# Kernel tuning notes

Measured on AMD Instinct MI355X. Metric: run time of the kernel, lower is better.

## Reference

```python
import jax, jax.numpy as jnp
import numpy as np
from jax import lax

B, C, H, W = 8, 384, 64, 64


def cos_map(N):
    # ortho DCT-II basis: weight[n, x] = cos(n*(x+0.5)*pi/N) * sqrt(2/N), row 0 /= sqrt(2)
    wx = (jnp.arange(N, dtype=jnp.float32) + 0.5) / N
    wn = jnp.arange(N, dtype=jnp.float32)[:, None]
    w = jnp.cos(wn * wx[None, :] * jnp.pi) * np.sqrt(2.0 / N).astype(np.float32)
    return w.at[0, :].multiply(np.float32(1.0 / np.sqrt(2.0)))


def setup_inputs() -> dict:
    key = jax.random.key(0)
    ks = jax.random.split(key, 8)
    s = 0.05
    return {
        "x": jax.random.normal(ks[0], (B, C, H, W), jnp.float32),
        "freq_embed": jax.random.normal(ks[1], (H, W, C), jnp.float32),
        "dw_w": jax.random.normal(ks[2], (C, 1, 3, 3), jnp.float32) * s,
        "dw_b": jnp.zeros((C,), jnp.float32),
        "lin_w": jax.random.normal(ks[3], (2 * C, C), jnp.float32) * s,
        "lin_b": jnp.zeros((2 * C,), jnp.float32),
        "tok_w": jax.random.normal(ks[4], (C, C), jnp.float32) * s,
        "tok_b": jnp.zeros((C,), jnp.float32),
        "c": jnp.ones((1,), jnp.float32),
        "alpha": jnp.ones((1,), jnp.float32) * 0.1,
        "ln_g": jnp.ones((C,), jnp.float32),
        "ln_b": jnp.zeros((C,), jnp.float32),
        "out_w": jax.random.normal(ks[5], (C, C), jnp.float32) * s,
        "out_b": jnp.zeros((C,), jnp.float32),
    }


def reference(x, freq_embed, dw_w, dw_b, lin_w, lin_b, tok_w, tok_b, c, alpha, ln_g, ln_b, out_w, out_b):
    Bc, Cc, Hc, Wc = x.shape
    # depthwise 3x3 conv
    x = lax.conv_general_dilated(x, dw_w, (1, 1), 'SAME',
                                 feature_group_count=Cc,
                                 dimension_numbers=('NCHW', 'OIHW', 'NCHW'))
    x = x + dw_b[None, :, None, None]
    # linear to 2C (channels-last), split into signal x and gate z
    xz = jnp.einsum('bchw,dc->bhwd', x, lin_w) + lin_b
    xs, z = xz[..., :Cc], xz[..., Cc:]          # [B,H,W,C]
    xs = jnp.transpose(xs, (0, 3, 1, 2))        # [B,C,H,W]
    # 2D ortho DCT-II: D = Wh @ x @ Ww^T
    Wh, Ww = cos_map(Hc), cos_map(Wc)
    Xd = jnp.einsum('nh,bchw,kw->bcnk', Wh, xs, Ww)
    # learned frequency gating: t = ReLU(Linear(freq_embed)), per (H,W,C)
    t = jax.nn.relu(jnp.einsum('hwc,dc->hwd', freq_embed, tok_w) + tok_b)
    ct = jnp.transpose(jnp.cos(c * t), (2, 0, 1))[None]        # [1,C,H,W]
    st = jnp.transpose(jnp.sin(c * t), (2, 0, 1))[None] / c[0]
    # x_u0 == x_v0 == Xd in the original (dct2d applied twice to same x)
    final = ct * Xd + st * (Xd + 0.5 * alpha[0] * Xd)
    # 2D inverse DCT: x = Wh^T @ D @ Ww
    xi = jnp.einsum('nh,bcnk,kw->bchw', Wh, final, Ww)
    # LayerNorm over channels, gate with SiLU(z), output linear
    y = jnp.transpose(xi, (0, 2, 3, 1))          # [B,H,W,C]
    mu = jnp.mean(y, axis=-1, keepdims=True)
    var = jnp.mean((y - mu) ** 2, axis=-1, keepdims=True)
    y = (y - mu) * lax.rsqrt(var + 1e-5) * ln_g + ln_b
    y = y * jax.nn.silu(z)
    y = jnp.einsum('bhwc,dc->bhwd', y, out_w) + out_b
    return jnp.transpose(y, (0, 3, 1, 2))        # [B,C,H,W]
```

## Files before the change

kernel.cpp:

```cpp
#include <hip/hip_runtime.h>

typedef _Float16 h2 __attribute__((ext_vector_type(2)));
typedef _Float16 h4 __attribute__((ext_vector_type(4)));
typedef _Float16 h8 __attribute__((ext_vector_type(8)));
typedef float    f4 __attribute__((ext_vector_type(4)));

#define MFMA32(a,b,c) __builtin_amdgcn_mfma_f32_16x16x32_f16((a),(b),(c),0,0,0)
#define MFMA16(a,b,c) __builtin_amdgcn_mfma_f32_16x16x16f16((a),(b),(c),0,0,0)

#define B_N 8
#define C_N 384
#define P_N 4096
#define PI_F 3.14159265358979323846f

__device__ __forceinline__ h4 to_h4(f4 v) {
  h4 r; r[0]=(_Float16)v[0]; r[1]=(_Float16)v[1]; r[2]=(_Float16)v[2]; r[3]=(_Float16)v[3];
  return r;
}

__device__ __forceinline__ void gl_lds16(const _Float16* g, _Float16* l) {
  __builtin_amdgcn_global_load_lds(
      (const __attribute__((address_space(1))) void*)g,
      (__attribute__((address_space(3))) void*)l, 16, 0, 0);
}

__global__ __launch_bounds__(256) void k_setup(
    const float* __restrict__ lin_w, const float* __restrict__ tok_w,
    const float* __restrict__ out_w, _Float16* __restrict__ lwh,
    _Float16* __restrict__ twh, _Float16* __restrict__ owh,
    _Float16* __restrict__ wmg, _Float16* __restrict__ wmtg) {
  int t = blockIdx.x * 256 + threadIdx.x;
  if (t < 768*384) lwh[t] = (_Float16)lin_w[t];
  if (t < 384*384) { twh[t] = (_Float16)tok_w[t]; owh[t] = (_Float16)out_w[t]; }
  if (t < 4096) {
    int n = t >> 6, h = t & 63;
    float v = cosf((float)n * ((float)h + 0.5f) * (PI_F / 64.0f)) * 0.1767766952966369f;
    if (n == 0) v *= 0.7071067811865476f;
    wmg[n*64 + h]  = (_Float16)v;
    wmtg[h*64 + n] = (_Float16)v;
  }
}

__global__ __launch_bounds__(256) void k_dwconv(
    const float* __restrict__ x, const float* __restrict__ dww,
    const float* __restrict__ dwb, _Float16* __restrict__ xdw) {
  int blk = blockIdx.x;
  int h = blk & 63;
  int rest = blk >> 6;
  int cgi = rest % 6;
  int b = rest / 6;
  int c0 = cgi * 64;
  int t = threadIdx.x;
  int w = t & 63, ci = t >> 6;
  __shared__ _Float16 buf[64 * 68];
  const float* xb = x + (size_t)b * C_N * P_N;
  int wl = (w > 0)  ? w - 1 : 0;
  int wr = (w < 63) ? w + 1 : 63;
  #pragma unroll
  for (int j = 0; j < 8; j++) {
    int lc = ci * 16 + j * 2;
    h2 pr;
    #pragma unroll
    for (int e = 0; e < 2; e++) {
      int c = c0 + lc + e;
      const float* xc = xb + (size_t)c * P_N;
      float k0=dww[c*9+0],k1=dww[c*9+1],k2=dww[c*9+2];
      float k3=dww[c*9+3],k4=dww[c*9+4],k5=dww[c*9+5];
      float k6=dww[c*9+6],k7=dww[c*9+7],k8=dww[c*9+8];
      float top = (h > 0)  ? xc[(h-1)*64 + w] : 0.0f;
      float mid = xc[h*64 + w];
      float bot = (h < 63) ? xc[(h+1)*64 + w] : 0.0f;
      float tl = __shfl(top, wl, 64), tr = __shfl(top, wr, 64);
      float ml = __shfl(mid, wl, 64), mr = __shfl(mid, wr, 64);
      float bl = __shfl(bot, wl, 64), br = __shfl(bot, wr, 64);
      if (w == 0)  { tl = 0.f; ml = 0.f; bl = 0.f; }
      if (w == 63) { tr = 0.f; mr = 0.f; br = 0.f; }
      float acc = dwb[c];
      acc += k0*tl + k1*top + k2*tr;
      acc += k3*ml + k4*mid + k5*mr;
      acc += k6*bl + k7*bot + k8*br;
      pr[e] = (_Float16)acc;
    }
    *(h2*)&buf[w*68 + lc] = pr;
  }
  __syncthreads();
  _Float16* op = xdw + ((size_t)b*P_N + h*64) * C_N + c0;
  #pragma unroll
  for (int i = 0; i < 4; i++) {
    int flat = (t + 256*i) * 4;
    int pix = flat >> 6, cl = flat & 63;
    *(h4*)&op[(size_t)pix*C_N + cl] = *(const h4*)&buf[pix*68 + cl];
  }
}

__global__ __launch_bounds__(256) void k_gate(
    const float* __restrict__ fe, const _Float16* __restrict__ twh,
    const float* __restrict__ tkb, const float* __restrict__ cc,
    const float* __restrict__ aa, _Float16* __restrict__ g) {
  int pt = blockIdx.x & 63, dt = blockIdx.x >> 6;
  int p0 = pt*64, d0 = dt*64;
  int t = threadIdx.x, lane = t & 63, wave = t >> 6;
  int quad = lane >> 4, l15 = lane & 15;
  int wm_ = wave >> 1, wn = wave & 1;
  __shared__ _Float16 la[64*40], lb[64*40];
  int srow = t >> 2, scg = (t & 3) * 8;
  f4 acc[2][2] = {};
  for (int kc = 0; kc < 384; kc += 32) {
    const float* src = fe + (size_t)(p0 + srow)*384 + kc + scg;
    f4 v0 = *(const f4*)src;
    f4 v1 = *(const f4*)(src + 4);
    h8 hv;
    hv[0]=(_Float16)v0[0]; hv[1]=(_Float16)v0[1]; hv[2]=(_Float16)v0[2]; hv[3]=(_Float16)v0[3];
    hv[4]=(_Float16)v1[0]; hv[5]=(_Float16)v1[1]; hv[6]=(_Float16)v1[2]; hv[7]=(_Float16)v1[3];
    *(h8*)&la[srow*40 + scg] = hv;
    *(h8*)&lb[srow*40 + scg] = *(const h8*)&twh[(size_t)(d0 + srow)*384 + kc + scg];
    __syncthreads();
    h8 a0 = *(const h8*)&la[(wm_*32 + l15)*40 + quad*8];
    h8 a1 = *(const h8*)&la[(wm_*32 + 16 + l15)*40 + quad*8];
    h8 b0 = *(const h8*)&lb[(wn*32 + l15)*40 + quad*8];
    h8 b1 = *(const h8*)&lb[(wn*32 + 16 + l15)*40 + quad*8];
    acc[0][0] = MFMA32(a0, b0, acc[0][0]);
    acc[0][1] = MFMA32(a0, b1, acc[0][1]);
    acc[1][0] = MFMA32(a1, b0, acc[1][0]);
    acc[1][1] = MFMA32(a1, b1, acc[1][1]);
    __syncthreads();
  }
  float c0 = cc[0];
  float s1 = (1.0f + 0.5f*aa[0]) / c0;
  #pragma unroll
  for (int i = 0; i < 2; i++)
  #pragma unroll
  for (int j = 0; j < 2; j++) {
    int d  = d0 + wn*32 + j*16 + l15;
    int pl = wm_*32 + i*16 + quad*4;
    float bias = tkb[d];
    h4 hv;
    #pragma unroll
    for (int r = 0; r < 4; r++) {
      float tv = fmaxf(acc[i][j][r] + bias, 0.0f);
      hv[r] = (_Float16)(__cosf(c0*tv) + s1*__sinf(c0*tv));
    }
    *(h4*)&g[(size_t)d*P_N + p0 + pl] = hv;
  }
}

__global__ __launch_bounds__(256) void k_gemm1(
    const _Float16* __restrict__ xdw, const _Float16* __restrict__ lwh,
    const float* __restrict__ lnb, _Float16* __restrict__ xs,
    _Float16* __restrict__ zs) {
  int pt = blockIdx.x & 31;
  int rest = blockIdx.x >> 5;
  int dt = rest % 6, b = rest / 6;
  int p0 = pt * 128, d0 = dt * 128;
  int t = threadIdx.x, lane = t & 63, wave = t >> 6;
  int quad = lane >> 4, l15 = lane & 15;
  int wm = wave >> 1, wn = wave & 1;
  __shared__ _Float16 la[128 * 32];
  __shared__ _Float16 lb[128 * 32];
  int s_row = lane >> 2;
  int s_col = (lane & 3) * 8;
  const _Float16* ga = xdw + ((size_t)b*P_N + p0) * 384 + s_col;
  const _Float16* gb = lwh + (size_t)d0 * 384 + s_col;
  f4 acc[4][4] = {};
  for (int kc = 0; kc < 384; kc += 32) {
    #pragma unroll
    for (int s = 0; s < 2; s++) {
      int seg = wave * 2 + s;
      int row = seg * 16 + s_row;
      gl_lds16(ga + (size_t)row*384 + kc, &la[seg*512 + lane*8]);
      gl_lds16(gb + (size_t)row*384 + kc, &lb[seg*512 + lane*8]);
    }
    __syncthreads();
    h8 af[4], bf[4];
    #pragma unroll
    for (int i = 0; i < 4; i++) {
      af[i] = *(const h8*)&la[(wm*64 + i*16 + l15)*32 + quad*8];
      bf[i] = *(const h8*)&lb[(wn*64 + i*16 + l15)*32 + quad*8];
    }
    #pragma unroll
    for (int i = 0; i < 4; i++)
    #pragma unroll
    for (int j = 0; j < 4; j++)
      acc[i][j] = MFMA32(af[i], bf[j], acc[i][j]);
    __syncthreads();
  }
  bool isz = (d0 >= 384);
  #pragma unroll
  for (int j = 0; j < 4; j++) {
    int d = d0 + wn*64 + j*16 + l15;
    float bias = lnb[d];
    _Float16* dst = isz ? (zs + ((size_t)b*C_N + (d-384)) * P_N)
                        : (xs + ((size_t)b*C_N + d) * P_N);
    #pragma unroll
    for (int i = 0; i < 4; i++) {
      int p = p0 + wm*64 + i*16 + quad*4;
      h4 hv;
      if (isz) {
        #pragma unroll
        for (int r = 0; r < 4; r++) {
          float v = acc[i][j][r] + bias;
          v = v / (1.0f + __expf(-v));
          hv[r] = (_Float16)v;
        }
      } else {
        #pragma unroll
        for (int r = 0; r < 4; r++) hv[r] = (_Float16)(acc[i][j][r] + bias);
      }
      *(h4*)&dst[p] = hv;
    }
  }
}

__global__ __launch_bounds__(256) void k_dct(
    const _Float16* __restrict__ xs, const _Float16* __restrict__ g,
    const _Float16* __restrict__ wmg, const _Float16* __restrict__ wmtg,
    _Float16* __restrict__ xi) {
  int b = blockIdx.x / 96, cg = blockIdx.x % 96;
  int c0 = cg * 4;
  int t = threadIdx.x, wave = t >> 6, lane = t & 63;
  int quad = lane >> 4, l15 = lane & 15;
  __shared__ _Float16 wm_s[64*72];
  __shared__ _Float16 wmt_s[64*72];
  __shared__ _Float16 pb[4][64*72];
  for (int i = t; i < 512; i += 256) {
    int row = i >> 3, col = (i & 7) * 8;
    *(h8*)&wm_s[row*72 + col]  = *(const h8*)&wmg[row*64 + col];
    *(h8*)&wmt_s[row*72 + col] = *(const h8*)&wmtg[row*64 + col];
  }
  const _Float16* xsb = xs + ((size_t)b*C_N + c0) * P_N;
  for (int i = t; i < 2048; i += 256) {
    int pl = i >> 9, idx = i & 511;
    int p = idx * 8, hh = p >> 6, ww = p & 63;
    *(h8*)&pb[pl][hh*72 + ww] = *(const h8*)&xsb[(size_t)pl*P_N + p];
  }
  __syncthreads();
  h8 aS[4][2], bW[4][2];
  #pragma unroll
  for (int I = 0; I < 4; I++)
  #pragma unroll
  for (int kk = 0; kk < 2; kk++) {
    aS[I][kk] = *(const h8*)&pb[wave][(I*16 + l15)*72 + kk*32 + quad*8];
    bW[I][kk] = *(const h8*)&wm_s[(I*16 + l15)*72 + kk*32 + quad*8];
  }
  h4 t1h[4][4];
  #pragma unroll
  for (int I = 0; I < 4; I++)
  #pragma unroll
  for (int J = 0; J < 4; J++) {
    f4 a = {};
    a = MFMA32(aS[I][0], bW[J][0], a);
    a = MFMA32(aS[I][1], bW[J][1], a);
    t1h[I][J] = to_h4(a);
  }
  __syncthreads();
  const _Float16* gb = g + (size_t)c0 * P_N;
  for (int i = t; i < 2048; i += 256) {
    int pl = i >> 9, idx = i & 511;
    int p = idx * 8, hh = p >> 6, ww = p & 63;
    *(h8*)&pb[pl][hh*72 + ww] = *(const h8*)&gb[(size_t)pl*P_N + p];
  }
  __syncthreads();
  f4 t2[4][4] = {};
  #pragma unroll
  for (int I = 0; I < 4; I++)
  #pragma unroll
  for (int K4 = 0; K4 < 4; K4++) {
    h4 af = *(const h4*)&wm_s[(I*16 + l15)*72 + K4*16 + quad*4];
    #pragma unroll
    for (int J = 0; J < 4; J++) t2[I][J] = MFMA16(af, t1h[K4][J], t2[I][J]);
  }
  h4 fh[4][4];
  #pragma unroll
  for (int I = 0; I < 4; I++)
  #pragma unroll
  for (int J = 0; J < 4; J++) {
    int n0 = I*16 + quad*4, k = J*16 + l15;
    h4 r;
    #pragma unroll
    for (int rr = 0; rr < 4; rr++) {
      float gv = (float)pb[wave][(n0+rr)*72 + k];
      r[rr] = (_Float16)(t2[I][J][rr] * gv);
    }
    fh[I][J] = r;
  }
  f4 t3[4][4] = {};
  #pragma unroll
  for (int J = 0; J < 4; J++)
  #pragma unroll
  for (int K4 = 0; K4 < 4; K4++) {
    h4 bf = *(const h4*)&wmt_s[(J*16 + l15)*72 + K4*16 + quad*4];
    #pragma unroll
    for (int I = 0; I < 4; I++) t3[I][J] = MFMA16(fh[K4][I], bf, t3[I][J]);
  }
  h4 t3h[4][4];
  #pragma unroll
  for (int I = 0; I < 4; I++)
  #pragma unroll
  for (int J = 0; J < 4; J++) t3h[I][J] = to_h4(t3[I][J]);
  f4 t4[4][4] = {};
  #pragma unroll
  for (int I = 0; I < 4; I++)
  #pragma unroll
  for (int K4 = 0; K4 < 4; K4++) {
    h4 af = *(const h4*)&wmt_s[(I*16 + l15)*72 + K4*16 + quad*4];
    #pragma unroll
    for (int J = 0; J < 4; J++) t4[I][J] = MFMA16(af, t3h[K4][J], t4[I][J]);
  }
  #pragma unroll
  for (int I = 0; I < 4; I++)
  #pragma unroll
  for (int J = 0; J < 4; J++) {
    int w0 = I*16 + quad*4, hq = J*16 + l15;
    *(h4*)&pb[wave][hq*72 + w0] = to_h4(t4[I][J]);
  }
  __syncthreads();
  _Float16* xib = xi + ((size_t)b*C_N + c0) * P_N;
  for (int i = t; i < 2048; i += 256) {
    int pl = i >> 9, idx = i & 511;
    int p = idx * 8, hh = p >> 6, ww = p & 63;
    *(h8*)&xib[(size_t)pl*P_N + p] = *(const h8*)&pb[pl][hh*72 + ww];
  }
}

__global__ __launch_bounds__(256) void k_ubuild(
    const _Float16* __restrict__ xi, const _Float16* __restrict__ zs,
    const float* __restrict__ lng, const float* __restrict__ lnbv,
    _Float16* __restrict__ u) {
  int b = blockIdx.x >> 6, pt = blockIdx.x & 63;
  int p0 = pt * 64;
  int t = threadIdx.x;
  __shared__ _Float16 ut[64 * 392];
  __shared__ float red[4][64], red2[4][64];
  __shared__ float muL[64], rsL[64];
  int cr = t >> 3;
  int px0 = (t & 7) * 8;
  const _Float16* xib = xi + (size_t)b * C_N * P_N;
  #pragma unroll
  for (int i = 0; i < 12; i++) {
    int c = cr + 32 * i;
    h8 v = *(const h8*)&xib[(size_t)c * P_N + p0 + px0];
    #pragma unroll
    for (int e = 0; e < 8; e++) ut[(px0 + e) * 392 + c] = v[e];
  }
  __syncthreads();
  int px = t & 63, seg = t >> 6;
  float s = 0.f, ss = 0.f;
  #pragma unroll
  for (int j = 0; j < 12; j++) {
    h8 v = *(const h8*)&ut[px * 392 + seg * 96 + j * 8];
    #pragma unroll
    for (int e = 0; e < 8; e++) { float f = (float)v[e]; s += f; ss += f * f; }
  }
  red[seg][px] = s; red2[seg][px] = ss;
  __syncthreads();
  if (t < 64) {
    float st  = red[0][t] + red[1][t] + red[2][t] + red[3][t];
    float sst = red2[0][t] + red2[1][t] + red2[2][t] + red2[3][t];
    float m = st * (1.f/384.f);
    float var = sst * (1.f/384.f) - m * m;
    muL[t] = m; rsL[t] = rsqrtf(var + 1e-5f);
  }
  __syncthreads();
  const _Float16* zb = zs + (size_t)b * C_N * P_N;
  #pragma unroll
  for (int i = 0; i < 12; i++) {
    int c = cr + 32 * i;
    float g = lng[c], bb = lnbv[c];
    h8 zv = *(const h8*)&zb[(size_t)c * P_N + p0 + px0];
    #pragma unroll
    for (int e = 0; e < 8; e++) {
      int p = px0 + e;
      float y = ((float)ut[p * 392 + c] - muL[p]) * rsL[p] * g + bb;
      ut[p * 392 + c] = (_Float16)(y * (float)zv[e]);
    }
  }
  __syncthreads();
  _Float16* ub = u + ((size_t)b * P_N + p0) * C_N;
  #pragma unroll
  for (int i = 0; i < 12; i++) {
    int idx = t + 256 * i;
    int row = idx / 48, ch = idx % 48;
    *(h8*)&ub[(size_t)row * C_N + ch * 8] = *(const h8*)&ut[row * 392 + ch * 8];
  }
}

__global__ __launch_bounds__(256) void k_gemm2(
    const _Float16* __restrict__ u, const _Float16* __restrict__ owh,
    const float* __restrict__ ob, float* __restrict__ out) {
  int pt = blockIdx.x & 31;
  int rest = blockIdx.x >> 5;
  int dt = rest % 3, b = rest / 3;
  int p0 = pt * 128, d0 = dt * 128;
  int t = threadIdx.x, lane = t & 63, wave = t >> 6;
  int quad = lane >> 4, l15 = lane & 15;
  int wm = wave >> 1, wn = wave & 1;
  __shared__ _Float16 la[128 * 32];
  __shared__ _Float16 lb[128 * 32];
  int s_row = lane >> 2;
  int s_col = (lane & 3) * 8;
  const _Float16* ga = u   + ((size_t)b*P_N + p0) * 384 + s_col;
  const _Float16* gb = owh + (size_t)d0 * 384 + s_col;
  f4 acc[4][4] = {};
  for (int kc = 0; kc < 384; kc += 32) {
    #pragma unroll
    for (int s = 0; s < 2; s++) {
      int seg = wave * 2 + s;
      int row = seg * 16 + s_row;
      gl_lds16(ga + (size_t)row*384 + kc, &la[seg*512 + lane*8]);
      gl_lds16(gb + (size_t)row*384 + kc, &lb[seg*512 + lane*8]);
    }
    __syncthreads();
    h8 af[4], bf[4];
    #pragma unroll
    for (int i = 0; i < 4; i++) {
      af[i] = *(const h8*)&la[(wm*64 + i*16 + l15)*32 + quad*8];
      bf[i] = *(const h8*)&lb[(wn*64 + i*16 + l15)*32 + quad*8];
    }
    #pragma unroll
    for (int i = 0; i < 4; i++)
    #pragma unroll
    for (int j = 0; j < 4; j++)
      acc[i][j] = MFMA32(af[i], bf[j], acc[i][j]);
    __syncthreads();
  }
  #pragma unroll
  for (int j = 0; j < 4; j++) {
    int d = d0 + wn*64 + j*16 + l15;
    float bias = ob[d];
    #pragma unroll
    for (int i = 0; i < 4; i++) {
      int p = p0 + wm*64 + i*16 + quad*4;
      f4 v;
      #pragma unroll
      for (int r = 0; r < 4; r++) v[r] = acc[i][j][r] + bias;
      *(f4*)&out[((size_t)b*C_N + d)*P_N + p] = v;
    }
  }
}

extern "C" void kernel_launch(void* const* d_in, const int* in_sizes, int n_in,
                              void* d_out, int out_size, void* d_ws, size_t ws_size,
                              hipStream_t stream) {
  (void)in_sizes; (void)n_in; (void)out_size; (void)ws_size;
  const float* x    = (const float*)d_in[0];
  const float* fe   = (const float*)d_in[1];
  const float* dww  = (const float*)d_in[2];
  const float* dwb  = (const float*)d_in[3];
  const float* linw = (const float*)d_in[4];
  const float* linb = (const float*)d_in[5];
  const float* tokw = (const float*)d_in[6];
  const float* tokb = (const float*)d_in[7];
  const float* cc   = (const float*)d_in[8];
  const float* aa   = (const float*)d_in[9];
  const float* lng  = (const float*)d_in[10];
  const float* lnbv = (const float*)d_in[11];
  const float* outw = (const float*)d_in[12];
  const float* outb = (const float*)d_in[13];
  float* out = (float*)d_out;

  char* ws = (char*)d_ws;
  size_t off = 0;
  auto alloc = [&](size_t bytes) -> void* {
    void* p = ws + off;
    off += (bytes + 255) & ~(size_t)255;
    return p;
  };
  _Float16* lwh  = (_Float16*)alloc((size_t)768*384*2);
  _Float16* twh  = (_Float16*)alloc((size_t)384*384*2);
  _Float16* owh  = (_Float16*)alloc((size_t)384*384*2);
  _Float16* wmg  = (_Float16*)alloc((size_t)64*64*2);
  _Float16* wmtg = (_Float16*)alloc((size_t)64*64*2);
  _Float16* xdw  = (_Float16*)alloc((size_t)B_N*P_N*C_N*2);
  _Float16* xs   = (_Float16*)alloc((size_t)B_N*C_N*P_N*2);
  _Float16* zs   = (_Float16*)alloc((size_t)B_N*C_N*P_N*2);
  _Float16* gg   = (_Float16*)alloc((size_t)C_N*P_N*2);
  _Float16* xi   = xdw;
  _Float16* uu   = xs;

  k_setup<<<1152, 256, 0, stream>>>(linw, tokw, outw, lwh, twh, owh, wmg, wmtg);
  k_dwconv<<<3072, 256, 0, stream>>>(x, dww, dwb, xdw);
  k_gate<<<384, 256, 0, stream>>>(fe, twh, tokb, cc, aa, gg);
  k_gemm1<<<1536, 256, 0, stream>>>(xdw, lwh, linb, xs, zs);
  k_dct<<<768, 256, 0, stream>>>(xs, gg, wmg, wmtg, xi);
  k_ubuild<<<512, 256, 0, stream>>>(xi, zs, lng, lnbv, uu);
  k_gemm2<<<768, 256, 0, stream>>>(uu, owh, outb, out);
}
```

Measured before the change: 259.9 us.

## Double-buffer LDS tiles in the two channel GEMMs to overlap loads with MFMA

The input-projection and output-projection GEMM kernels now use two LDS buffer pairs and prefetch the next K-slice via global_load_lds while running MFMAs on the current one. This cuts the per-iteration barrier count from two to one and hides global-load latency behind compute. It doubles LDS usage per block (32 KB), which can lower occupancy, and correctness depends on the vmcnt waits the compiler emits before the barrier.

```diff
diff --git a/kernel.cpp b/kernel.cpp
--- a/kernel.cpp
+++ b/kernel.cpp
@@ -22,6 +22,35 @@
   __builtin_amdgcn_global_load_lds(
       (const __attribute__((address_space(1))) void*)g,
       (__attribute__((address_space(3))) void*)l, 16, 0, 0);
+}
+
+__device__ __forceinline__ void gemm_step(
+    const _Float16* __restrict__ ga, const _Float16* __restrict__ gb,
+    int kc, bool pref,
+    _Float16* laC, _Float16* lbC, _Float16* laN, _Float16* lbN,
+    int wave, int s_row, int wm, int wn, int l15, int quad, f4 (&acc)[4][4]) {
+  if (pref) {
+    #pragma unroll
+    for (int s = 0; s < 2; s++) {
+      int seg = wave * 2 + s;
+      int row = seg * 16 + s_row;
+      int lane = (threadIdx.x & 63);
+      gl_lds16(ga + (size_t)row*384 + kc + 32, &laN[seg*512 + lane*8]);
+      gl_lds16(gb + (size_t)row*384 + kc + 32, &lbN[seg*512 + lane*8]);
+    }
+  }
+  h8 af[4], bf[4];
+  #pragma unroll
+  for (int i = 0; i < 4; i++) {
+    af[i] = *(const h8*)&laC[(wm*64 + i*16 + l15)*32 + quad*8];
+    bf[i] = *(const h8*)&lbC[(wn*64 + i*16 + l15)*32 + quad*8];
+  }
+  #pragma unroll
+  for (int i = 0; i < 4; i++)
+  #pragma unroll
+  for (int j = 0; j < 4; j++)
+    acc[i][j] = MFMA32(af[i], bf[j], acc[i][j]);
+  __syncthreads();
 }
 
 __global__ __launch_bounds__(256) void k_setup(
@@ -155,34 +184,28 @@
   int t = threadIdx.x, lane = t & 63, wave = t >> 6;
   int quad = lane >> 4, l15 = lane & 15;
   int wm = wave >> 1, wn = wave & 1;
-  __shared__ _Float16 la[128 * 32];
-  __shared__ _Float16 lb[128 * 32];
+  __shared__ _Float16 la0[128 * 32], lb0[128 * 32];
+  __shared__ _Float16 la1[128 * 32], lb1[128 * 32];
   int s_row = lane >> 2;
   int s_col = (lane & 3) * 8;
   const _Float16* ga = xdw + ((size_t)b*P_N + p0) * 384 + s_col;
   const _Float16* gb = lwh + (size_t)d0 * 384 + s_col;
   f4 acc[4][4] = {};
-  for (int kc = 0; kc < 384; kc += 32) {
-    #pragma unroll
-    for (int s = 0; s < 2; s++) {
-      int seg = wave * 2 + s;
-      int row = seg * 16 + s_row;
-      gl_lds16(ga + (size_t)row*384 + kc, &la[seg*512 + lane*8]);
-      gl_lds16(gb + (size_t)row*384 + kc, &lb[seg*512 + lane*8]);
-    }
-    __syncthreads();
-    h8 af[4], bf[4];
-    #pragma unroll
-    for (int i = 0; i < 4; i++) {
-      af[i] = *(const h8*)&la[(wm*64 + i*16 + l15)*32 + quad*8];
-      bf[i] = *(const h8*)&lb[(wn*64 + i*16 + l15)*32 + quad*8];
-    }
-    #pragma unroll
-    for (int i = 0; i < 4; i++)
-    #pragma unroll
-    for (int j = 0; j < 4; j++)
-      acc[i][j] = MFMA32(af[i], bf[j], acc[i][j]);
-    __syncthreads();
+  #pragma unroll
+  for (int s = 0; s < 2; s++) {
+    int seg = wave * 2 + s;
+    int row = seg * 16 + s_row;
+    gl_lds16(ga + (size_t)row*384, &la0[seg*512 + lane*8]);
+    gl_lds16(gb + (size_t)row*384, &lb0[seg*512 + lane*8]);
+  }
+  __syncthreads();
+  #pragma unroll
+  for (int kt = 0; kt < 6; kt++) {
+    int kc = kt * 64;
+    gemm_step(ga, gb, kc,      true,            la0, lb0, la1, lb1,
+              wave, s_row, wm, wn, l15, quad, acc);
+    gemm_step(ga, gb, kc + 32, (kc + 64 < 384), la1, lb1, la0, lb0,
+              wave, s_row, wm, wn, l15, quad, acc);
   }
   bool isz = (d0 >= 384);
   #pragma unroll
@@ -394,34 +417,28 @@
   int t = threadIdx.x, lane = t & 63, wave = t >> 6;
   int quad = lane >> 4, l15 = lane & 15;
   int wm = wave >> 1, wn = wave & 1;
-  __shared__ _Float16 la[128 * 32];
-  __shared__ _Float16 lb[128 * 32];
+  __shared__ _Float16 la0[128 * 32], lb0[128 * 32];
+  __shared__ _Float16 la1[128 * 32], lb1[128 * 32];
   int s_row = lane >> 2;
   int s_col = (lane & 3) * 8;
   const _Float16* ga = u   + ((size_t)b*P_N + p0) * 384 + s_col;
   const _Float16* gb = owh + (size_t)d0 * 384 + s_col;
   f4 acc[4][4] = {};
-  for (int kc = 0; kc < 384; kc += 32) {
-    #pragma unroll
-    for (int s = 0; s < 2; s++) {
-      int seg = wave * 2 + s;
-      int row = seg * 16 + s_row;
-      gl_lds16(ga + (size_t)row*384 + kc, &la[seg*512 + lane*8]);
-      gl_lds16(gb + (size_t)row*384 + kc, &lb[seg*512 + lane*8]);
-    }
-    __syncthreads();
-    h8 af[4], bf[4];
-    #pragma unroll
-    for (int i = 0; i < 4; i++) {
-      af[i] = *(const h8*)&la[(wm*64 + i*16 + l15)*32 + quad*8];
-      bf[i] = *(const h8*)&lb[(wn*64 + i*16 + l15)*32 + quad*8];
-    }
-    #pragma unroll
-    for (int i = 0; i < 4; i++)
-    #pragma unroll
-    for (int j = 0; j < 4; j++)
-      acc[i][j] = MFMA32(af[i], bf[j], acc[i][j]);
-    __syncthreads();
+  #pragma unroll
+  for (int s = 0; s < 2; s++) {
+    int seg = wave * 2 + s;
+    int row = seg * 16 + s_row;
+    gl_lds16(ga + (size_t)row*384, &la0[seg*512 + lane*8]);
+    gl_lds16(gb + (size_t)row*384, &lb0[seg*512 + lane*8]);
+  }
+  __syncthreads();
+  #pragma unroll
+  for (int kt = 0; kt < 6; kt++) {
+    int kc = kt * 64;
+    gemm_step(ga, gb, kc,      true,            la0, lb0, la1, lb1,
+              wave, s_row, wm, wn, l15, quad, acc);
+    gemm_step(ga, gb, kc + 32, (kc + 64 < 384), la1, lb1, la0, lb0,
+              wave, s_row, wm, wn, l15, quad, acc);
   }
   #pragma unroll
   for (int j = 0; j < 4; j++) {
```

Measured after the change: 258.7 us. Within noise of the previous version (-0.4%).

## Double-buffer K=64 LDS staging and use 8-wave blocks in both GEMMs

Applied to the files above, without the earlier changes.

Both pointwise GEMM kernels now run with 512 threads (8 waves, each owning a 32x64 sub-tile) instead of 256. They stage K in chunks of 64 into two ping-pong LDS buffers, so the next chunk's global-to-LDS load is issued before the MFMAs on the current chunk. This halves the number of barriers and is meant to hide global load latency behind MFMA work. The cost is four times the LDS per block (64 KB), which limits how many blocks fit per CU, and fewer accumulators per wave.

```diff
diff --git a/kernel.cpp b/kernel.cpp
--- a/kernel.cpp
+++ b/kernel.cpp
@@ -22,6 +22,44 @@
   __builtin_amdgcn_global_load_lds(
       (const __attribute__((address_space(1))) void*)g,
       (__attribute__((address_space(3))) void*)l, 16, 0, 0);
+}
+
+__device__ __forceinline__ void stage64(const _Float16* g, _Float16* lds) {
+  int lane = threadIdx.x & 63, wave = threadIdx.x >> 6;
+  int row = wave * 16 + (lane >> 2);
+  #pragma unroll
+  for (int r = 0; r < 2; r++) {
+    gl_lds16(g + (size_t)row * 384 + r * 32, lds + r * 4096 + wave * 512 + lane * 8);
+  }
+}
+
+__device__ __forceinline__ void gstep64(
+    const _Float16* __restrict__ ga, const _Float16* __restrict__ gb,
+    int kcn, bool pref,
+    const _Float16* laC, const _Float16* lbC,
+    _Float16* laN, _Float16* lbN, f4 (&acc)[2][4]) {
+  int lane = threadIdx.x & 63, wave = threadIdx.x >> 6;
+  int quad = lane >> 4, l15 = lane & 15;
+  int wm = wave >> 1, wn = wave & 1;
+  if (pref) { stage64(ga + kcn, laN); stage64(gb + kcn, lbN); }
+  h8 af[2][2], bf[4][2];
+  #pragma unroll
+  for (int kk = 0; kk < 2; kk++) {
+    #pragma unroll
+    for (int i = 0; i < 2; i++)
+      af[i][kk] = *(const h8*)&laC[kk*4096 + (wm*32 + i*16 + l15)*32 + quad*8];
+    #pragma unroll
+    for (int j = 0; j < 4; j++)
+      bf[j][kk] = *(const h8*)&lbC[kk*4096 + (wn*64 + j*16 + l15)*32 + quad*8];
+  }
+  #pragma unroll
+  for (int kk = 0; kk < 2; kk++)
+  #pragma unroll
+  for (int i = 0; i < 2; i++)
+  #pragma unroll
+  for (int j = 0; j < 4; j++)
+    acc[i][j] = MFMA32(af[i][kk], bf[j][kk], acc[i][j]);
+  __syncthreads();
 }
 
 __global__ __launch_bounds__(256) void k_setup(
@@ -144,7 +182,7 @@
   }
 }
 
-__global__ __launch_bounds__(256) void k_gemm1(
+__global__ __launch_bounds__(512, 4) void k_gemm1(
     const _Float16* __restrict__ xdw, const _Float16* __restrict__ lwh,
     const float* __restrict__ lnb, _Float16* __restrict__ xs,
     _Float16* __restrict__ zs) {
@@ -155,34 +193,18 @@
   int t = threadIdx.x, lane = t & 63, wave = t >> 6;
   int quad = lane >> 4, l15 = lane & 15;
   int wm = wave >> 1, wn = wave & 1;
-  __shared__ _Float16 la[128 * 32];
-  __shared__ _Float16 lb[128 * 32];
-  int s_row = lane >> 2;
-  int s_col = (lane & 3) * 8;
-  const _Float16* ga = xdw + ((size_t)b*P_N + p0) * 384 + s_col;
-  const _Float16* gb = lwh + (size_t)d0 * 384 + s_col;
-  f4 acc[4][4] = {};
-  for (int kc = 0; kc < 384; kc += 32) {
-    #pragma unroll
-    for (int s = 0; s < 2; s++) {
-      int seg = wave * 2 + s;
-      int row = seg * 16 + s_row;
-      gl_lds16(ga + (size_t)row*384 + kc, &la[seg*512 + lane*8]);
-      gl_lds16(gb + (size_t)row*384 + kc, &lb[seg*512 + lane*8]);
-    }
-    __syncthreads();
-    h8 af[4], bf[4];
-    #pragma unroll
-    for (int i = 0; i < 4; i++) {
-      af[i] = *(const h8*)&la[(wm*64 + i*16 + l15)*32 + quad*8];
-      bf[i] = *(const h8*)&lb[(wn*64 + i*16 + l15)*32 + quad*8];
-    }
-    #pragma unroll
-    for (int i = 0; i < 4; i++)
-    #pragma unroll
-    for (int j = 0; j < 4; j++)
-      acc[i][j] = MFMA32(af[i], bf[j], acc[i][j]);
-    __syncthreads();
+  __shared__ _Float16 la0[2*128*32], lb0[2*128*32];
+  __shared__ _Float16 la1[2*128*32], lb1[2*128*32];
+  const _Float16* ga = xdw + ((size_t)b*P_N + p0) * 384 + (lane & 3) * 8;
+  const _Float16* gb = lwh + (size_t)d0 * 384 + (lane & 3) * 8;
+  f4 acc[2][4] = {};
+  stage64(ga, la0); stage64(gb, lb0);
+  __syncthreads();
+  #pragma unroll
+  for (int kt = 0; kt < 3; kt++) {
+    int kc = kt * 128;
+    gstep64(ga, gb, kc + 64,  true,            la0, lb0, la1, lb1, acc);
+    gstep64(ga, gb, kc + 128, (kc + 128 < 384), la1, lb1, la0, lb0, acc);
   }
   bool isz = (d0 >= 384);
   #pragma unroll
@@ -192,8 +214,8 @@
     _Float16* dst = isz ? (zs + ((size_t)b*C_N + (d-384)) * P_N)
                         : (xs + ((size_t)b*C_N + d) * P_N);
     #pragma unroll
-    for (int i = 0; i < 4; i++) {
-      int p = p0 + wm*64 + i*16 + quad*4;
+    for (int i = 0; i < 2; i++) {
+      int p = p0 + wm*32 + i*16 + quad*4;
       h4 hv;
       if (isz) {
         #pragma unroll
@@ -384,7 +406,7 @@
   }
 }
 
-__global__ __launch_bounds__(256) void k_gemm2(
+__global__ __launch_bounds__(512, 4) void k_gemm2(
     const _Float16* __restrict__ u, const _Float16* __restrict__ owh,
     const float* __restrict__ ob, float* __restrict__ out) {
   int pt = blockIdx.x & 31;
@@ -394,42 +416,26 @@
   int t = threadIdx.x, lane = t & 63, wave = t >> 6;
   int quad = lane >> 4, l15 = lane & 15;
   int wm = wave >> 1, wn = wave & 1;
-  __shared__ _Float16 la[128 * 32];
-  __shared__ _Float16 lb[128 * 32];
-  int s_row = lane >> 2;
-  int s_col = (lane & 3) * 8;
-  const _Float16* ga = u   + ((size_t)b*P_N + p0) * 384 + s_col;
-  const _Float16* gb = owh + (size_t)d0 * 384 + s_col;
-  f4 acc[4][4] = {};
-  for (int kc = 0; kc < 384; kc += 32) {
-    #pragma unroll
-    for (int s = 0; s < 2; s++) {
-      int seg = wave * 2 + s;
-      int row = seg * 16 + s_row;
-      gl_lds16(ga + (size_t)row*384 + kc, &la[seg*512 + lane*8]);
-      gl_lds16(gb + (size_t)row*384 + kc, &lb[seg*512 + lane*8]);
-    }
-    __syncthreads();
-    h8 af[4], bf[4];
-    #pragma unroll
-    for (int i = 0; i < 4; i++) {
-      af[i] = *(const h8*)&la[(wm*64 + i*16 + l15)*32 + quad*8];
-      bf[i] = *(const h8*)&lb[(wn*64 + i*16 + l15)*32 + quad*8];
-    }
-    #pragma unroll
-    for (int i = 0; i < 4; i++)
-    #pragma unroll
-    for (int j = 0; j < 4; j++)
-      acc[i][j] = MFMA32(af[i], bf[j], acc[i][j]);
-    __syncthreads();
+  __shared__ _Float16 la0[2*128*32], lb0[2*128*32];
+  __shared__ _Float16 la1[2*128*32], lb1[2*128*32];
+  const _Float16* ga = u   + ((size_t)b*P_N + p0) * 384 + (lane & 3) * 8;
+  const _Float16* gb = owh + (size_t)d0 * 384 + (lane & 3) * 8;
+  f4 acc[2][4] = {};
+  stage64(ga, la0); stage64(gb, lb0);
+  __syncthreads();
+  #pragma unroll
+  for (int kt = 0; kt < 3; kt++) {
+    int kc = kt * 128;
+    gstep64(ga, gb, kc + 64,  true,            la0, lb0, la1, lb1, acc);
+    gstep64(ga, gb, kc + 128, (kc + 128 < 384), la1, lb1, la0, lb0, acc);
   }
   #pragma unroll
   for (int j = 0; j < 4; j++) {
     int d = d0 + wn*64 + j*16 + l15;
     float bias = ob[d];
     #pragma unroll
-    for (int i = 0; i < 4; i++) {
-      int p = p0 + wm*64 + i*16 + quad*4;
+    for (int i = 0; i < 2; i++) {
+      int p = p0 + wm*32 + i*16 + quad*4;
       f4 v;
       #pragma unroll
       for (int r = 0; r < 4; r++) v[r] = acc[i][j][r] + bias;
@@ -480,8 +486,8 @@
   k_setup<<<1152, 256, 0, stream>>>(linw, tokw, outw, lwh, twh, owh, wmg, wmtg);
   k_dwconv<<<3072, 256, 0, stream>>>(x, dww, dwb, xdw);
   k_gate<<<384, 256, 0, stream>>>(fe, twh, tokb, cc, aa, gg);
-  k_gemm1<<<1536, 256, 0, stream>>>(xdw, lwh, linb, xs, zs);
+  k_gemm1<<<1536, 512, 0, stream>>>(xdw, lwh, linb, xs, zs);
   k_dct<<<768, 256, 0, stream>>>(xs, gg, wmg, wmtg, xi);
   k_ubuild<<<512, 256, 0, stream>>>(xi, zs, lng, lnbv, uu);
-  k_gemm2<<<768, 256, 0, stream>>>(uu, owh, outb, out);
-}
+  k_gemm2<<<768, 512, 0, stream>>>(uu, owh, outb, out);
+}
```

After: 253.4 us. 1.03x faster.
